# Kernel tuning notes

Measured on AMD Instinct MI355X. Metric: run time of the kernel, lower is better.

Reference implementation:

```python
import jax, jax.numpy as jnp
import numpy as np

T = 8192      # sequence length (scan steps)
D_IN = 1024   # input feature dim
H = 1024      # d_model (hidden size)


def setup_inputs() -> dict:
    key = jax.random.key(0)
    k1, k2, k3, k4 = jax.random.split(key, 4)
    inputs = jax.random.normal(k1, (T, D_IN), dtype=jnp.float32)
    terminations = jax.random.randint(k2, (T,), 0, 2) > 0  # bool [T]
    last_state = jnp.zeros((H,), dtype=jnp.float32)
    # GRUCell params (flax layout: input kernel with bias for all 3 gates;
    # recurrent kernel, bias only on the candidate 'n' gate).
    # Gate order within the 3H axis: [r, z, n].
    Wi = jax.random.normal(k3, (D_IN, 3 * H), dtype=jnp.float32) / np.sqrt(D_IN)
    bi = jnp.zeros((3 * H,), dtype=jnp.float32)
    Wh = jax.random.normal(k4, (H, 3 * H), dtype=jnp.float32) / np.sqrt(H)
    bhn = jnp.zeros((H,), dtype=jnp.float32)
    return {"inputs": inputs, "terminations": terminations, "last_state": last_state,
            "Wi": Wi, "bi": bi, "Wh": Wh, "bhn": bhn}


def reference(inputs, terminations, last_state, Wi, bi, Wh, bhn):
    # Precompute all input-side gate preactivations in one big GEMM: [T, 3H]
    gi_all = inputs @ Wi + bi

    def step(h, xs):
        gi, term = xs
        # reset_on_terminate: zero the carry when the episode terminated
        h = jnp.where(term, jnp.zeros_like(h), h)
        gh = h @ Wh                      # [3H], recurrent preactivations
        gi_r, gi_z, gi_n = jnp.split(gi, 3)
        gh_r, gh_z, gh_n = jnp.split(gh, 3)
        r = jax.nn.sigmoid(gi_r + gh_r)
        z = jax.nn.sigmoid(gi_z + gh_z)
        n = jnp.tanh(gi_n + r * (gh_n + bhn))
        h_new = (1.0 - z) * n + z * h    # flax GRUCell update
        # GRUout emits (new_c, (new_c, new_h)); flax GRUCell returns new_h twice
        return h_new, (h_new, h_new)

    _, (new_states, y_t) = jax.lax.scan(step, last_state, (gi_all, terminations))
    return (y_t, new_states)  # each [T, H]
```

## Files before the change

kernel.cpp:

```cpp
#include <hip/hip_runtime.h>
#include <stdint.h>

#define T_LEN 8192
#define DIN   1024
#define HD    1024
#define TH    3072
#define NB    16
#define SKINNY_MAX 160

typedef __attribute__((ext_vector_type(8))) short bf16x8;
typedef __attribute__((ext_vector_type(4))) float f32x4;

__device__ __forceinline__ unsigned short f2bf(float x) {
    union { float f; unsigned u; } v; v.f = x;
    unsigned r = v.u + 0x7FFFu + ((v.u >> 16) & 1u);
    return (unsigned short)(r >> 16);
}

__device__ __forceinline__ void gld16(const void* g, void* l) {
    __builtin_amdgcn_global_load_lds(
        (const __attribute__((address_space(1))) unsigned int*)(uintptr_t)g,
        (__attribute__((address_space(3))) unsigned int*)(uintptr_t)l,
        16, 0, 0);
}

__device__ __forceinline__ float sigm(float x) { return 1.f / (1.f + __expf(-x)); }
__device__ __forceinline__ float tanh_fast(float x) { return 1.f - 2.f / (1.f + __expf(2.f * x)); }

__global__ void cast_x(const float* __restrict__ X, unsigned short* __restrict__ Xb) {
    int idx = (blockIdx.x * 256 + threadIdx.x) * 4;
    float4 v = *(const float4*)(X + idx);
    ushort4 o; o.x = f2bf(v.x); o.y = f2bf(v.y); o.z = f2bf(v.z); o.w = f2bf(v.w);
    *(ushort4*)(Xb + idx) = o;
}

__global__ void transpose_cast(const float* __restrict__ Wi, const float* __restrict__ Wh,
                               unsigned short* __restrict__ WiT, unsigned short* __restrict__ WhT) {
    const float* src = blockIdx.z ? Wh : Wi;
    unsigned short* dst = blockIdx.z ? WhT : WiT;
    int n0 = blockIdx.x * 64, k0 = blockIdx.y * 64;
    __shared__ unsigned short tile[64][65];
    int tid = threadIdx.x;
    for (int p = 0; p < 16; p++) {
        int idx = tid + p * 256;
        int kl = idx >> 6, nl = idx & 63;
        tile[kl][nl] = f2bf(src[(size_t)(k0 + kl) * TH + n0 + nl]);
    }
    __syncthreads();
    for (int p = 0; p < 16; p++) {
        int idx = tid + p * 256;
        int nl = idx >> 6, kl = idx & 63;
        dst[(size_t)(n0 + nl) * 1024 + k0 + kl] = tile[kl][nl];
    }
}

__global__ void meta_kernel(const int* __restrict__ term, const float* __restrict__ last_state,
                            int* __restrict__ pos_list, int* __restrict__ meta) {
    __shared__ int part[1024];
    __shared__ int cnt[NB];
    __shared__ int cur[NB];
    __shared__ int flag;
    int tid = threadIdx.x;
    if (tid < NB) cnt[tid] = 0;
    if (tid == 0) flag = 0;
    __syncthreads();
    int base = tid * 8;
    int mx = -1;
    for (int u = 0; u < 8; u++) {
        int t = base + u;
        int s = (t == 0 || term[t] != 0) ? t : -1;
        mx = s > mx ? s : mx;
    }
    part[tid] = mx;
    __syncthreads();
    for (int d = 1; d < 1024; d <<= 1) {
        int a = part[tid];
        int b = (tid >= d) ? part[tid - d] : -1;
        __syncthreads();
        part[tid] = a > b ? a : b;
        __syncthreads();
    }
    int run = (tid > 0) ? part[tid - 1] : -1;
    int kk[8];
    for (int u = 0; u < 8; u++) {
        int t = base + u;
        int s = (t == 0 || term[t] != 0) ? t : -1;
        run = s > run ? s : run;
        int ls = t - run;
        int k = ls < NB ? ls : NB - 1;
        kk[u] = k;
        atomicAdd(&cnt[k], 1);
    }
    if (last_state[tid] != 0.0f) atomicOr(&flag, 1);
    __syncthreads();
    if (tid == 0) {
        int off = 0;
        for (int k = 0; k < NB; k++) {
            meta[k] = cnt[k];
            meta[NB + k] = off;
            cur[k] = off;
            off += cnt[k];
        }
        meta[2 * NB] = flag;
    }
    __syncthreads();
    for (int u = 0; u < 8; u++) {
        int idx = atomicAdd(&cur[kk[u]], 1);
        pos_list[idx] = base + u;
    }
}

__global__ __launch_bounds__(256) void gemm_gi(const unsigned short* __restrict__ Xb,
                                               const unsigned short* __restrict__ WiT,
                                               const float* __restrict__ bi,
                                               float* __restrict__ gi) {
    __shared__ unsigned short As[128 * 32];
    __shared__ unsigned short Bs[128 * 32];
    int tid = threadIdx.x;
    int m0 = blockIdx.y * 128, n0 = blockIdx.x * 128;
    int lane = tid & 63, wave = tid >> 6;
    int wm = wave & 1, wn = wave >> 1;
    int quad = lane >> 4, l16 = lane & 15;
    f32x4 acc[4][4] = {};
    for (int kb = 0; kb < 32; kb++) {
        int k0 = kb * 32;
        for (int p = 0; p < 2; p++) {
            int c = tid + p * 256;
            int row = c >> 2, cb = c & 3;
            gld16(Xb + (size_t)(m0 + row) * 1024 + k0 + cb * 8, As + c * 8);
            gld16(WiT + (size_t)(n0 + row) * 1024 + k0 + cb * 8, Bs + c * 8);
        }
        __syncthreads();
        bf16x8 af[4], bfr[4];
        for (int i = 0; i < 4; i++)
            af[i] = *(const bf16x8*)(As + (wm * 64 + i * 16 + l16) * 32 + quad * 8);
        for (int j = 0; j < 4; j++)
            bfr[j] = *(const bf16x8*)(Bs + (wn * 64 + j * 16 + l16) * 32 + quad * 8);
        for (int i = 0; i < 4; i++)
            for (int j = 0; j < 4; j++)
                acc[i][j] = __builtin_amdgcn_mfma_f32_16x16x32_bf16(af[i], bfr[j], acc[i][j], 0, 0, 0);
        __syncthreads();
    }
    for (int j = 0; j < 4; j++) {
        int col = n0 + wn * 64 + j * 16 + l16;
        float bv = bi[col];
        for (int i = 0; i < 4; i++) {
            int rbase = m0 + wm * 64 + i * 16 + quad * 4;
            for (int r = 0; r < 4; r++)
                gi[(size_t)(rbase + r) * TH + col] = acc[i][j][r] + bv;
        }
    }
}

__global__ void pass0_kernel(const float* __restrict__ gi, const float* __restrict__ bhn,
                             const float* __restrict__ last_state, const float* __restrict__ Wh,
                             const int* __restrict__ term, const int* __restrict__ pos_list,
                             const int* __restrict__ meta, float* __restrict__ out,
                             unsigned short* __restrict__ hb) {
    int S0 = meta[0];
    int b = blockIdx.x;
    if (b >= S0) return;
    int t = pos_list[meta[NB] + b];
    int tid = threadIdx.x;
    bool ls_path = (t == 0) && (term[0] == 0) && (meta[2 * NB] != 0);
    for (int u = 0; u < 4; u++) {
        int j = tid + u * 256;
        float gr = gi[(size_t)t * TH + j];
        float gz = gi[(size_t)t * TH + 1024 + j];
        float gn = gi[(size_t)t * TH + 2048 + j];
        float hp = 0.f, ghr = 0.f, ghz = 0.f, ghn = 0.f;
        if (ls_path) {
            hp = last_state[j];
            for (int k = 0; k < 1024; k++) {
                float hk = last_state[k];
                const float* w = Wh + (size_t)k * TH;
                ghr += hk * w[j]; ghz += hk * w[1024 + j]; ghn += hk * w[2048 + j];
            }
        }
        float r = sigm(gr + ghr);
        float z = sigm(gz + ghz);
        float n = tanh_fast(gn + r * (ghn + bhn[j]));
        float h = (1.f - z) * n + z * hp;
        out[(size_t)t * HD + j] = h;
        out[(size_t)(T_LEN + t) * HD + j] = h;
        hb[(size_t)t * HD + j] = f2bf(h);
    }
}

__global__ __launch_bounds__(256) void pass_gemm(const float* __restrict__ gi,
                                                 const float* __restrict__ bhn,
                                                 const unsigned short* __restrict__ WhT,
                                                 const unsigned short* __restrict__ hb,
                                                 float* __restrict__ out,
                                                 unsigned short* __restrict__ hbw,
                                                 const int* __restrict__ pos_list,
                                                 const int* __restrict__ meta, int k) {
    int S = meta[k];
    int off = meta[NB + k];
    int tid = threadIdx.x;
    int lane = tid & 63, wave = tid >> 6;
    int quad = lane >> 4, l16 = lane & 15;

    if (S <= SKINNY_MAX) {
        if (S == 0) return;
        int nrt = (S + 15) >> 4;
        int ntask = 64 * nrt;
        int gwave = ((blockIdx.y * 16 + blockIdx.x) << 2) + wave;
        int nw = gridDim.x * gridDim.y * 4;
        for (int task = gwave; task < ntask; task += nw) {
            int ct = task & 63;
            int rt = task >> 6;
            int j = ct * 16 + l16;
            int ra = rt * 16 + l16;
            ra = ra < S ? ra : S - 1;
            int t_a = pos_list[off + ra];
            const unsigned short* ap = hb + (size_t)(t_a - 1) * HD + quad * 8;
            const unsigned short* bp = WhT + (size_t)j * 1024 + quad * 8;
            f32x4 acc[3] = {};
            #pragma unroll
            for (int ks = 0; ks < 32; ks++) {
                bf16x8 a  = *(const bf16x8*)(ap + ks * 32);
                bf16x8 b0 = *(const bf16x8*)(bp + ks * 32);
                bf16x8 b1 = *(const bf16x8*)(bp + 1048576 + ks * 32);
                bf16x8 b2 = *(const bf16x8*)(bp + 2097152 + ks * 32);
                acc[0] = __builtin_amdgcn_mfma_f32_16x16x32_bf16(a, b0, acc[0], 0, 0, 0);
                acc[1] = __builtin_amdgcn_mfma_f32_16x16x32_bf16(a, b1, acc[1], 0, 0, 0);
                acc[2] = __builtin_amdgcn_mfma_f32_16x16x32_bf16(a, b2, acc[2], 0, 0, 0);
            }
            #pragma unroll
            for (int r = 0; r < 4; r++) {
                int rr = rt * 16 + quad * 4 + r;
                if (rr >= S) continue;
                int t = pos_list[off + rr];
                const float* girow = gi + (size_t)t * TH;
                float hp = out[(size_t)(t - 1) * HD + j];
                float rgt = sigm(girow[j] + acc[0][r]);
                float zgt = sigm(girow[1024 + j] + acc[1][r]);
                float ngt = tanh_fast(girow[2048 + j] + rgt * (acc[2][r] + bhn[j]));
                float hv = (1.f - zgt) * ngt + zgt * hp;
                out[(size_t)t * HD + j] = hv;
                out[(size_t)(T_LEN + t) * HD + j] = hv;
                hbw[(size_t)t * HD + j] = f2bf(hv);
            }
        }
        return;
    }

    int r0 = blockIdx.y * 64;
    if (r0 >= S) return;
    int j0 = blockIdx.x * 64;
    __shared__ unsigned short As[4 * 64 * 32];
    __shared__ unsigned short Bs[4 * 192 * 32];
    int wm = wave & 1, wn = wave >> 1;

    int arow = tid >> 2, sub = tid & 3;
    bool av = (r0 + arow) < S;
    int t_a = av ? pos_list[off + r0 + arow] : 1;
    const unsigned short* hsrc = hb + (size_t)(t_a - 1) * HD + sub * 8;

    f32x4 acc[2][6] = {};
    for (int kb = 0; kb < 8; kb++) {
        int k0 = kb * 128;
        for (int ks = 0; ks < 4; ks++) {
            int kk0 = k0 + ks * 32;
            for (int p = 0; p < 3; p++) {
                int c = tid + p * 256;
                int row = c >> 2, q = c & 3;
                int g = row >> 6, jj = row & 63;
                gld16(WhT + (size_t)(g * 1024 + j0 + jj) * 1024 + kk0 + q * 8,
                      Bs + ks * 6144 + c * 8);
            }
            gld16(hsrc + kk0, As + ks * 2048 + tid * 8);
        }
        __syncthreads();
        for (int ks = 0; ks < 4; ks++) {
            bf16x8 af[2];
            for (int i = 0; i < 2; i++)
                af[i] = *(const bf16x8*)(As + ks * 2048 + (wm * 32 + i * 16 + l16) * 32 + quad * 8);
            for (int n = 0; n < 6; n++) {
                int g = n >> 1, jh = n & 1;
                bf16x8 bv = *(const bf16x8*)(Bs + ks * 6144 + (g * 64 + wn * 32 + jh * 16 + l16) * 32 + quad * 8);
                for (int i = 0; i < 2; i++)
                    acc[i][n] = __builtin_amdgcn_mfma_f32_16x16x32_bf16(af[i], bv, acc[i][n], 0, 0, 0);
            }
        }
        __syncthreads();
    }
    for (int i = 0; i < 2; i++) {
        for (int r = 0; r < 4; r++) {
            int rr = r0 + wm * 32 + i * 16 + quad * 4 + r;
            if (rr >= S) continue;
            int t = pos_list[off + rr];
            const float* girow = gi + (size_t)t * TH;
            const float* hprow = out + (size_t)(t - 1) * HD;
            float* o1 = out + (size_t)t * HD;
            float* o2 = out + (size_t)(T_LEN + t) * HD;
            unsigned short* hbrow = hbw + (size_t)t * HD;
            for (int jh = 0; jh < 2; jh++) {
                int j = j0 + wn * 32 + jh * 16 + l16;
                float ghr = acc[i][0 + jh][r];
                float ghz = acc[i][2 + jh][r];
                float ghn = acc[i][4 + jh][r];
                float rg = sigm(girow[j] + ghr);
                float zg = sigm(girow[1024 + j] + ghz);
                float ng = tanh_fast(girow[2048 + j] + rg * (ghn + bhn[j]));
                float h = (1.f - zg) * ng + zg * hprow[j];
                o1[j] = h;
                o2[j] = h;
                hbrow[j] = f2bf(h);
            }
        }
    }
}

__global__ void tail_kernel(const float* __restrict__ gi, const float* __restrict__ bhn,
                            const float* __restrict__ Wh,
                            const int* __restrict__ pos_list, const int* __restrict__ meta,
                            float* __restrict__ out) {
    __shared__ int pos[T_LEN];
    int S = meta[NB - 1];
    if (S == 0) return;
    int off = meta[NB + NB - 1];
    int tid = threadIdx.x;
    for (int i = tid; i < S; i += 256) pos[i] = pos_list[off + i];
    __syncthreads();
    if (tid == 0) {
        for (int i = 1; i < S; i++) {
            int v = pos[i], j = i - 1;
            while (j >= 0 && pos[j] > v) { pos[j + 1] = pos[j]; j--; }
            pos[j + 1] = v;
        }
    }
    __syncthreads();
    for (int s = 0; s < S; s++) {
        int t = pos[s];
        const float* hp = out + (size_t)(t - 1) * HD;
        const float* girow = gi + (size_t)t * TH;
        float hv[4];
        for (int c = 0; c < 4; c++) {
            int j = tid * 4 + c;
            float ghr = 0.f, ghz = 0.f, ghn = 0.f;
            for (int kk = 0; kk < 1024; kk++) {
                float hk = hp[kk];
                const float* w = Wh + (size_t)kk * TH;
                ghr += hk * w[j]; ghz += hk * w[1024 + j]; ghn += hk * w[2048 + j];
            }
            float rg = sigm(girow[j] + ghr);
            float zg = sigm(girow[1024 + j] + ghz);
            float ng = tanh_fast(girow[2048 + j] + rg * (ghn + bhn[j]));
            hv[c] = (1.f - zg) * ng + zg * hp[j];
        }
        __syncthreads();
        for (int c = 0; c < 4; c++) {
            int j = tid * 4 + c;
            out[(size_t)t * HD + j] = hv[c];
            out[(size_t)(T_LEN + t) * HD + j] = hv[c];
        }
        __syncthreads();
    }
}

extern "C" void kernel_launch(void* const* d_in, const int* in_sizes, int n_in,
                              void* d_out, int out_size, void* d_ws, size_t ws_size,
                              hipStream_t stream) {
    const float* X          = (const float*)d_in[0];
    const int*   term       = (const int*)d_in[1];
    const float* last_state = (const float*)d_in[2];
    const float* Wi         = (const float*)d_in[3];
    const float* bi         = (const float*)d_in[4];
    const float* Wh         = (const float*)d_in[5];
    const float* bhn        = (const float*)d_in[6];
    float* out = (float*)d_out;

    char* ws = (char*)d_ws;
    float*          gi       = (float*)ws;
    unsigned short* Xb       = (unsigned short*)(ws + 100663296);
    unsigned short* hb       = Xb;
    unsigned short* WiT      = (unsigned short*)(ws + 117440512);
    unsigned short* WhT      = (unsigned short*)(ws + 123731968);
    int*            pos_list = (int*)(ws + 130023424);
    int*            meta     = (int*)(ws + 130056192);

    cast_x<<<dim3(8192), dim3(256), 0, stream>>>(X, Xb);
    transpose_cast<<<dim3(48, 16, 2), dim3(256), 0, stream>>>(Wi, Wh, WiT, WhT);
    meta_kernel<<<dim3(1), dim3(1024), 0, stream>>>(term, last_state, pos_list, meta);
    gemm_gi<<<dim3(24, 64), dim3(256), 0, stream>>>(Xb, WiT, bi, gi);
    pass0_kernel<<<dim3(8192), dim3(256), 0, stream>>>(gi, bhn, last_state, Wh, term, pos_list, meta, out, hb);
    for (int k = 1; k < NB - 1; k++) {
        int rows_max = T_LEN / (k + 1);
        int gy = (rows_max + 63) / 64;
        pass_gemm<<<dim3(16, gy), dim3(256), 0, stream>>>(gi, bhn, WhT, hb, out, hb, pos_list, meta, k);
    }
    tail_kernel<<<dim3(1), dim3(256), 0, stream>>>(gi, bhn, Wh, pos_list, meta, out);
}
```

Before: 431.8 us.

## Spread tail recurrence across 16 cooperative blocks and deepen input GEMM K-tile

The serial tail of the scan, which handles the remaining steps whose chain runs longer than the batched passes cover, used to run on a single block that read fp32 Wh column-wise. It now runs as a cooperative kernel over 16 blocks. Each block computes 64 output columns per step from bf16 transposed Wh with vectorized loads, and the blocks meet at a grid sync after every step. Separately, the input-projection GEMM K tile grows from 32 to 64, halving the barrier count at the cost of more LDS. Using bf16 Wh in the tail adds precision loss there, and each step now pays a grid-sync cost.

```diff
diff --git a/kernel.cpp b/kernel.cpp
--- a/kernel.cpp
+++ b/kernel.cpp
@@ -1,4 +1,5 @@
 #include <hip/hip_runtime.h>
+#include <hip/hip_cooperative_groups.h>
 #include <stdint.h>
 
 #define T_LEN 8192
@@ -8,6 +9,8 @@
 #define NB    16
 #define SKINNY_MAX 160
 
+namespace coop = cooperative_groups;
+
 typedef __attribute__((ext_vector_type(8))) short bf16x8;
 typedef __attribute__((ext_vector_type(4))) float f32x4;
 
@@ -15,6 +18,11 @@
     union { float f; unsigned u; } v; v.f = x;
     unsigned r = v.u + 0x7FFFu + ((v.u >> 16) & 1u);
     return (unsigned short)(r >> 16);
+}
+
+__device__ __forceinline__ float bf2f(unsigned short x) {
+    union { unsigned u; float f; } v; v.u = ((unsigned)x) << 16;
+    return v.f;
 }
 
 __device__ __forceinline__ void gld16(const void* g, void* l) {
@@ -114,31 +122,33 @@
                                                const unsigned short* __restrict__ WiT,
                                                const float* __restrict__ bi,
                                                float* __restrict__ gi) {
-    __shared__ unsigned short As[128 * 32];
-    __shared__ unsigned short Bs[128 * 32];
+    __shared__ unsigned short As[128 * 64];
+    __shared__ unsigned short Bs[128 * 64];
     int tid = threadIdx.x;
     int m0 = blockIdx.y * 128, n0 = blockIdx.x * 128;
     int lane = tid & 63, wave = tid >> 6;
     int wm = wave & 1, wn = wave >> 1;
     int quad = lane >> 4, l16 = lane & 15;
     f32x4 acc[4][4] = {};
-    for (int kb = 0; kb < 32; kb++) {
-        int k0 = kb * 32;
-        for (int p = 0; p < 2; p++) {
+    for (int kb = 0; kb < 16; kb++) {
+        int k0 = kb * 64;
+        for (int p = 0; p < 4; p++) {
             int c = tid + p * 256;
-            int row = c >> 2, cb = c & 3;
+            int row = c >> 3, cb = c & 7;
             gld16(Xb + (size_t)(m0 + row) * 1024 + k0 + cb * 8, As + c * 8);
             gld16(WiT + (size_t)(n0 + row) * 1024 + k0 + cb * 8, Bs + c * 8);
         }
         __syncthreads();
-        bf16x8 af[4], bfr[4];
-        for (int i = 0; i < 4; i++)
-            af[i] = *(const bf16x8*)(As + (wm * 64 + i * 16 + l16) * 32 + quad * 8);
-        for (int j = 0; j < 4; j++)
-            bfr[j] = *(const bf16x8*)(Bs + (wn * 64 + j * 16 + l16) * 32 + quad * 8);
-        for (int i = 0; i < 4; i++)
+        for (int ks = 0; ks < 2; ks++) {
+            bf16x8 af[4], bfr[4];
+            for (int i = 0; i < 4; i++)
+                af[i] = *(const bf16x8*)(As + (wm * 64 + i * 16 + l16) * 64 + ks * 32 + quad * 8);
             for (int j = 0; j < 4; j++)
-                acc[i][j] = __builtin_amdgcn_mfma_f32_16x16x32_bf16(af[i], bfr[j], acc[i][j], 0, 0, 0);
+                bfr[j] = *(const bf16x8*)(Bs + (wn * 64 + j * 16 + l16) * 64 + ks * 32 + quad * 8);
+            for (int i = 0; i < 4; i++)
+                for (int j = 0; j < 4; j++)
+                    acc[i][j] = __builtin_amdgcn_mfma_f32_16x16x32_bf16(af[i], bfr[j], acc[i][j], 0, 0, 0);
+        }
         __syncthreads();
     }
     for (int j = 0; j < 4; j++) {
@@ -313,15 +323,20 @@
     }
 }
 
-__global__ void tail_kernel(const float* __restrict__ gi, const float* __restrict__ bhn,
-                            const float* __restrict__ Wh,
-                            const int* __restrict__ pos_list, const int* __restrict__ meta,
-                            float* __restrict__ out) {
-    __shared__ int pos[T_LEN];
+__global__ __launch_bounds__(256) void tail_coop(const float* __restrict__ gi,
+                                                 const float* __restrict__ bhn,
+                                                 const unsigned short* __restrict__ WhT,
+                                                 const int* __restrict__ pos_list,
+                                                 const int* __restrict__ meta,
+                                                 float* __restrict__ out) {
     int S = meta[NB - 1];
     if (S == 0) return;
+    __shared__ int pos[T_LEN];
+    __shared__ float hsh[HD];
+    __shared__ float dots[192];
     int off = meta[NB + NB - 1];
     int tid = threadIdx.x;
+    int j0 = blockIdx.x * 64;
     for (int i = tid; i < S; i += 256) pos[i] = pos_list[off + i];
     __syncthreads();
     if (tid == 0) {
@@ -332,31 +347,40 @@
         }
     }
     __syncthreads();
+    coop::grid_group grid = coop::this_grid();
     for (int s = 0; s < S; s++) {
         int t = pos[s];
-        const float* hp = out + (size_t)(t - 1) * HD;
-        const float* girow = gi + (size_t)t * TH;
-        float hv[4];
-        for (int c = 0; c < 4; c++) {
-            int j = tid * 4 + c;
-            float ghr = 0.f, ghz = 0.f, ghn = 0.f;
-            for (int kk = 0; kk < 1024; kk++) {
-                float hk = hp[kk];
-                const float* w = Wh + (size_t)kk * TH;
-                ghr += hk * w[j]; ghz += hk * w[1024 + j]; ghn += hk * w[2048 + j];
-            }
-            float rg = sigm(girow[j] + ghr);
-            float zg = sigm(girow[1024 + j] + ghz);
-            float ng = tanh_fast(girow[2048 + j] + rg * (ghn + bhn[j]));
-            hv[c] = (1.f - zg) * ng + zg * hp[j];
-        }
-        __syncthreads();
-        for (int c = 0; c < 4; c++) {
-            int j = tid * 4 + c;
-            out[(size_t)t * HD + j] = hv[c];
-            out[(size_t)(T_LEN + t) * HD + j] = hv[c];
-        }
-        __syncthreads();
+        for (int u = 0; u < 4; u++)
+            hsh[tid + u * 256] = out[(size_t)(t - 1) * HD + tid + u * 256];
+        __syncthreads();
+        if (tid < 192) {
+            int g = tid >> 6, jj = tid & 63;
+            int col = g * 1024 + j0 + jj;
+            const unsigned short* wrow = WhT + (size_t)col * 1024;
+            float acc = 0.f;
+            for (int kk = 0; kk < 1024; kk += 8) {
+                bf16x8 wv = *(const bf16x8*)(wrow + kk);
+                f32x4 h0 = *(const f32x4*)(hsh + kk);
+                f32x4 h1 = *(const f32x4*)(hsh + kk + 4);
+                acc += h0[0] * bf2f((unsigned short)wv[0]) + h0[1] * bf2f((unsigned short)wv[1])
+                     + h0[2] * bf2f((unsigned short)wv[2]) + h0[3] * bf2f((unsigned short)wv[3])
+                     + h1[0] * bf2f((unsigned short)wv[4]) + h1[1] * bf2f((unsigned short)wv[5])
+                     + h1[2] * bf2f((unsigned short)wv[6]) + h1[3] * bf2f((unsigned short)wv[7]);
+            }
+            dots[tid] = acc;
+        }
+        __syncthreads();
+        if (tid < 64) {
+            int j = j0 + tid;
+            float rg = sigm(gi[(size_t)t * TH + j] + dots[tid]);
+            float zg = sigm(gi[(size_t)t * TH + 1024 + j] + dots[64 + tid]);
+            float ng = tanh_fast(gi[(size_t)t * TH + 2048 + j] + rg * (dots[128 + tid] + bhn[j]));
+            float hv = (1.f - zg) * ng + zg * hsh[j];
+            out[(size_t)t * HD + j] = hv;
+            out[(size_t)(T_LEN + t) * HD + j] = hv;
+        }
+        __threadfence();
+        grid.sync();
     }
 }
 
@@ -391,5 +415,10 @@
         int gy = (rows_max + 63) / 64;
         pass_gemm<<<dim3(16, gy), dim3(256), 0, stream>>>(gi, bhn, WhT, hb, out, hb, pos_list, meta, k);
     }
-    tail_kernel<<<dim3(1), dim3(256), 0, stream>>>(gi, bhn, Wh, pos_list, meta, out);
-}
+    {
+        void* args[] = { (void*)&gi, (void*)&bhn, (void*)&WhT,
+                         (void*)&pos_list, (void*)&meta, (void*)&out };
+        hipLaunchCooperativeKernel((void*)tail_coop, dim3(16), dim3(256),
+                                   args, 0, stream);
+    }
+}
```

Result: slower. 487.2 us (+12.8%).
